# Performance work log

Measured on AMD Instinct MI355X. Metric: run time of the kernel, lower is better.

Reference implementation:

```python
import jax, jax.numpy as jnp
import numpy as np

VERY_NEG = -100000000000.0
EPS = 1e-10
PAGERANK_LAMBDA = 0.8
FACT_SCALE = 1.0
B, E, F, LQ = 64, 1000, 4000, 30
T = 100      # trans_units
EMB = 300    # embed_units
WV = 30000   # word vocab
EV = 50007   # entity vocab (+7 specials)
GNN_LAYERS = 2


def linear(x, W, b):
    return x @ W.T + b


def lstm(x, Wih, Whh, bih, bhh):
    # torch nn.LSTM, single layer, batch_first. gate order i,f,g,o
    Bb = x.shape[0]
    H = Whh.shape[1]
    def step(carry, xt):
        h, c = carry
        g = xt @ Wih.T + h @ Whh.T + bih + bhh
        i, f, gg, o = jnp.split(g, 4, axis=-1)
        c = jax.nn.sigmoid(f) * c + jax.nn.sigmoid(i) * jnp.tanh(gg)
        h = jax.nn.sigmoid(o) * jnp.tanh(c)
        return (h, c), h
    init = (jnp.zeros((Bb, H), x.dtype), jnp.zeros((Bb, H), x.dtype))
    (h, _), ys = jax.lax.scan(step, init, jnp.swapaxes(x, 0, 1))
    return jnp.swapaxes(ys, 0, 1), h


def gather_entity(x, head_idx):
    # sparse_bmm(entity2fact_mat, x): each fact row has one nonzero at its head entity
    # x [B,E,D], head_idx [B,F] -> [B,F,D]
    return jnp.take_along_axis(x, head_idx[:, :, None], axis=1)


def scatter_fact(y, tail_idx):
    # sparse_bmm(fact2entity_mat, y): scatter-add fact rows into their tail entity
    # y [B,F,D], tail_idx [B,F] -> [B,E,D]
    Bb, Ff, D = y.shape
    seg = (jnp.arange(Bb)[:, None] * E + tail_idx).reshape(-1)
    return jax.ops.segment_sum(y.reshape(Bb * Ff, D), seg, num_segments=Bb * E).reshape(Bb, E, D)


def forward(word_emb, entity_emb, ent_W, ent_b, lstm_Wih, lstm_Whh, lstm_bih, lstm_bhh,
            q2e_W, q2e_b, e2q_W, e2q_b, e2e_W, e2e_b,
            kbh_W, kbh_b, kbt_W, kbt_b, kbs_W, kbs_b,
            q2e_adj_mat, query_text, local_entity, kb_fact_rel, head_idx, tail_idx):
    div = jnp.sqrt(jnp.asarray(T, jnp.float32))
    query_mask = (query_text != 0).astype(jnp.float32)          # [B,LQ]

    # node encoder (LSTM) over query words
    qw = word_emb[query_text]                                   # [B,LQ,EMB]
    query_hidden_emb, qh = lstm(qw, lstm_Wih, lstm_Whh, lstm_bih, lstm_bhh)
    query_node_emb = qh[:, None, :]                             # [B,1,T]

    local_fact_emb = linear(entity_emb[kb_fact_rel], ent_W, ent_b)     # [B,F,T]
    local_entity_emb = linear(entity_emb[local_entity], ent_W, ent_b)  # [B,E,T]

    # fact <-> query attention (pre-GNN weighting)
    sim = jnp.einsum('blt,bft->blf', query_hidden_emb, local_fact_emb) / div
    sim = jax.nn.softmax(sim + (1.0 - query_mask[:, :, None]) * VERY_NEG, axis=1)
    fact2query_att = jnp.einsum('blf,blt->bft', sim, query_hidden_emb)  # [B,F,T]
    Wsc = jnp.sum(fact2query_att * local_fact_emb, axis=2) / div        # [B,F]
    W_tilde = jnp.exp(Wsc - jnp.max(Wsc, axis=1, keepdims=True))        # [B,F]

    # e2f_softmax = entity2fact^T @ W_tilde : per-entity sum of W_tilde over out-facts
    e2f_softmax = scatter_fact(W_tilde[:, :, None], head_idx)[:, :, 0]
    e2f_softmax = jnp.maximum(e2f_softmax, EPS)                         # [B,E]

    pagerank_f = q2e_adj_mat                                            # [B,E]
    for i in range(GNN_LAYERS):
        next_emb = local_entity_emb
        # question -> entity
        q2e = linear(jnp.broadcast_to(query_node_emb, (B, E, T)), q2e_W[i], q2e_b[i])
        next_emb = jnp.concatenate([next_emb, q2e], axis=2)
        # entity -> fact
        e2f_emb = jax.nn.relu(linear(local_fact_emb, kbs_W[i], kbs_b[i]) +
                              gather_entity(linear(local_entity_emb, kbh_W[i], kbh_b[i]), head_idx))
        e2f_norm = W_tilde[:, :, None] * gather_entity((pagerank_f / e2f_softmax)[:, :, None], head_idx)
        e2f_emb = e2f_emb * e2f_norm                                    # [B,F,T]
        # fact -> entity
        f2e_emb = jax.nn.relu(linear(local_entity_emb, kbs_W[i], kbs_b[i]) +
                              scatter_fact(linear(e2f_emb, kbt_W[i], kbt_b[i]), tail_idx))
        pagerank_f = (PAGERANK_LAMBDA * scatter_fact(e2f_norm, tail_idx)[:, :, 0] +
                      (1.0 - PAGERANK_LAMBDA) * pagerank_f)
        next_emb = jnp.concatenate([next_emb, FACT_SCALE * f2e_emb], axis=2)  # [B,E,3T]
        # entity -> query ; entity -> entity
        query_node_emb = jnp.einsum('be,bet->bt', pagerank_f,
                                    linear(next_emb, e2q_W[i], e2q_b[i]))[:, None, :]
        local_entity_emb = jax.nn.relu(linear(next_emb, e2e_W[i], e2e_b[i]))
    return local_entity_emb, query_node_emb, pagerank_f


def setup_inputs() -> dict:
    key = jax.random.key(0)
    ks = jax.random.split(key, 24)
    def n(k, shape, s=0.05):
        return (jax.random.normal(k, shape) * s).astype(jnp.float32)
    L, K3 = GNN_LAYERS, 3 * T
    inp = {}
    inp['word_emb'] = n(ks[0], (WV, EMB), 1.0)
    inp['entity_emb'] = n(ks[1], (EV, T), 1.0)
    inp['ent_W'] = n(ks[2], (T, T)); inp['ent_b'] = jnp.zeros((T,), jnp.float32)
    inp['lstm_Wih'] = n(ks[3], (4 * T, EMB)); inp['lstm_Whh'] = n(ks[4], (4 * T, T))
    inp['lstm_bih'] = jnp.zeros((4 * T,), jnp.float32)
    inp['lstm_bhh'] = jnp.zeros((4 * T,), jnp.float32)
    inp['q2e_W'] = n(ks[5], (L, T, T)); inp['q2e_b'] = jnp.zeros((L, T), jnp.float32)
    inp['e2q_W'] = n(ks[6], (L, T, K3)); inp['e2q_b'] = jnp.zeros((L, T), jnp.float32)
    inp['e2e_W'] = n(ks[7], (L, T, K3)); inp['e2e_b'] = jnp.zeros((L, T), jnp.float32)
    inp['kbh_W'] = n(ks[8], (L, T, T)); inp['kbh_b'] = jnp.zeros((L, T), jnp.float32)
    inp['kbt_W'] = n(ks[9], (L, T, T)); inp['kbt_b'] = jnp.zeros((L, T), jnp.float32)
    inp['kbs_W'] = n(ks[10], (L, T, T)); inp['kbs_b'] = jnp.zeros((L, T), jnp.float32)
    inp['q2e_adj_mat'] = (jax.random.uniform(ks[11], (B, E)) < 0.05).astype(jnp.float32)
    inp['query_text'] = jax.random.randint(ks[12], (B, LQ), 0, WV)
    inp['local_entity'] = jax.random.randint(ks[13], (B, E), 0, EV)
    inp['kb_fact_rel'] = jax.random.randint(ks[14], (B, F), 0, EV)
    inp['head_idx'] = jax.random.randint(ks[15], (B, F), 0, E)
    inp['tail_idx'] = jax.random.randint(ks[16], (B, F), 0, E)
    return inp


def reference(word_emb, entity_emb, ent_W, ent_b, lstm_Wih, lstm_Whh, lstm_bih, lstm_bhh,
              q2e_W, q2e_b, e2q_W, e2q_b, e2e_W, e2e_b,
              kbh_W, kbh_b, kbt_W, kbt_b, kbs_W, kbs_b,
              q2e_adj_mat, query_text, local_entity, kb_fact_rel, head_idx, tail_idx):
    return forward(word_emb, entity_emb, ent_W, ent_b, lstm_Wih, lstm_Whh, lstm_bih, lstm_bhh,
                   q2e_W, q2e_b, e2q_W, e2q_b, e2e_W, e2e_b,
                   kbh_W, kbh_b, kbt_W, kbt_b, kbs_W, kbs_b,
                   q2e_adj_mat, query_text, local_entity, kb_fact_rel, head_idx, tail_idx)
```

## Files before the change

kernel.cpp:

```cpp
#include <hip/hip_runtime.h>
#include <hip/hip_bf16.h>

#define BB 64
#define EE 1000
#define FF 4000
#define LQ_ 30
#define TT 100
#define EMB_ 300
#define G4 400
#define EV_ 50007
#define VERY_NEG_ (-100000000000.0f)
#define EPS_ 1e-10f

typedef __attribute__((ext_vector_type(8))) short bf16x8;
typedef __attribute__((ext_vector_type(4))) float f32x4;

__device__ __forceinline__ float sigm(float x) { return 1.0f / (1.0f + expf(-x)); }

__device__ __forceinline__ unsigned short f2bf(float v) {
    __hip_bfloat16 h = __float2bfloat16(v);
    return *reinterpret_cast<unsigned short*>(&h);
}
__device__ __forceinline__ float bf2f(unsigned short s) {
    return __uint_as_float((unsigned)s << 16);
}

__global__ void cvt_bf16_kernel(const float* __restrict__ in, unsigned short* __restrict__ out,
                                long n4) {
    long i = (long)blockIdx.x * 256 + threadIdx.x;
    if (i < n4) {
        float4 v = ((const float4*)in)[i];
        ushort4 o;
        o.x = f2bf(v.x); o.y = f2bf(v.y); o.z = f2bf(v.z); o.w = f2bf(v.w);
        ((ushort4*)out)[i] = o;
    }
}

__global__ void transpose_kernel(const float* __restrict__ in, float* __restrict__ out,
                                 int rows, int cols) {
    int i = blockIdx.x * 256 + threadIdx.x;
    if (i < rows * cols) {
        int r = i / cols, c = i % cols;
        out[c * rows + r] = in[i];
    }
}

__global__ __launch_bounds__(256)
void xw_kernel(const float* __restrict__ word_emb, const int* __restrict__ qtext,
               const float* __restrict__ WihT, const float* __restrict__ bih,
               const float* __restrict__ bhh, float* __restrict__ xw) {
    int bs0 = blockIdx.x * 4;
    __shared__ float x[4][EMB_];
    int tid = threadIdx.x;
    for (int i = tid; i < 4 * EMB_; i += 256) {
        int s = i / EMB_, k = i % EMB_;
        x[s][k] = word_emb[(long)qtext[bs0 + s] * EMB_ + k];
    }
    __syncthreads();
    for (int g = tid; g < G4; g += 256) {
        float b0 = bih[g] + bhh[g];
        float a0 = b0, a1 = b0, a2 = b0, a3 = b0;
        #pragma unroll 4
        for (int k = 0; k < EMB_; ++k) {
            float wv = WihT[k * G4 + g];
            a0 += x[0][k] * wv; a1 += x[1][k] * wv;
            a2 += x[2][k] * wv; a3 += x[3][k] * wv;
        }
        xw[(long)(bs0 + 0) * G4 + g] = a0;
        xw[(long)(bs0 + 1) * G4 + g] = a1;
        xw[(long)(bs0 + 2) * G4 + g] = a2;
        xw[(long)(bs0 + 3) * G4 + g] = a3;
    }
}

__global__ __launch_bounds__(512)
void lstm_kernel(const float* __restrict__ xw, const float* __restrict__ Whh,
                 float* __restrict__ qh_emb, float* __restrict__ qnode) {
    int b = blockIdx.x, tid = threadIdx.x;
    __shared__ __align__(16) float hs[TT];
    __shared__ float cs[TT];
    __shared__ float gs[G4];
    float4 w[25];
    if (tid < G4) {
        const float4* wr = (const float4*)(Whh + (long)tid * TT);
        #pragma unroll
        for (int j = 0; j < 25; ++j) w[j] = wr[j];
    }
    if (tid < TT) { hs[tid] = 0.f; cs[tid] = 0.f; }
    __syncthreads();
    for (int s = 0; s < LQ_; ++s) {
        if (tid < G4) {
            const float4* hv4 = (const float4*)hs;
            float a0 = 0.f, a1 = 0.f, a2 = 0.f, a3 = 0.f;
            #pragma unroll
            for (int j = 0; j < 25; ++j) {
                float4 hv = hv4[j];
                a0 += hv.x * w[j].x; a1 += hv.y * w[j].y;
                a2 += hv.z * w[j].z; a3 += hv.w * w[j].w;
            }
            gs[tid] = xw[((long)b * LQ_ + s) * G4 + tid] + (a0 + a1) + (a2 + a3);
        }
        __syncthreads();
        if (tid < TT) {
            float ci = sigm(gs[TT + tid]) * cs[tid] + sigm(gs[tid]) * tanhf(gs[2 * TT + tid]);
            float hi = sigm(gs[3 * TT + tid]) * tanhf(ci);
            cs[tid] = ci;
            hs[tid] = hi;
            qh_emb[((long)b * LQ_ + s) * TT + tid] = hi;
            if (s == LQ_ - 1) qnode[b * TT + tid] = hi;
        }
        __syncthreads();
    }
}

struct GOut {
    const float* W; int wstride;
    const float* bias;
    const float* bscale;
    const unsigned short* addb;
    const float* addf;
    const float* cvec;
    void* Y; int y_bf16; int relu;
};
struct GArgs {
    const void* X; int x_bf16;
    const int* gidx;
    long rows;
    int nw;
    GOut o[3];
};

__global__ __launch_bounds__(256)
void gemm_multi_kernel(GArgs a) {
    __shared__ __align__(16) short sX[64 * 136];
    __shared__ __align__(16) short sW[112 * 136];
    float* sOut = (float*)sW;
    int tid = threadIdx.x;
    long r0 = (long)blockIdx.x * 64;
    for (int i = tid; i < 64 * 25; i += 256) {
        int r = i / 25, c = i % 25;
        long rr = r0 + r;
        ushort4 v; v.x = 0; v.y = 0; v.z = 0; v.w = 0;
        if (rr < a.rows) {
            long xr = a.gidx ? (long)a.gidx[rr] : rr;
            if (a.x_bf16) {
                v = *(const ushort4*)((const unsigned short*)a.X + xr * TT + c * 4);
            } else {
                float4 f = *(const float4*)((const float*)a.X + xr * TT + c * 4);
                v.x = f2bf(f.x); v.y = f2bf(f.y); v.z = f2bf(f.z); v.w = f2bf(f.w);
            }
        }
        *(ushort4*)&sX[r * 136 + c * 4] = v;
    }
    for (int i = tid; i < 64 * 28; i += 256) {
        int r = i / 28, k = TT + i % 28;
        sX[r * 136 + k] = 0;
    }
    int lane = tid & 63, wv = tid >> 6;
    int arow = lane & 15, agrp = lane >> 4;
    int t_lo = lane & 15, r_hi = (lane >> 4) * 4;
    #pragma unroll
    for (int w = 0; w < 3; ++w) {
        if (w >= a.nw) break;
        for (int i = tid; i < 112 * 32; i += 256) {
            int t = i / 32, k = (i % 32) * 4;
            ushort4 v; v.x = 0; v.y = 0; v.z = 0; v.w = 0;
            if (t < TT && k < TT) {
                float4 f = *(const float4*)(a.o[w].W + (long)t * a.o[w].wstride + k);
                v.x = f2bf(f.x); v.y = f2bf(f.y); v.z = f2bf(f.z); v.w = f2bf(f.w);
            }
            *(ushort4*)&sW[t * 136 + k] = v;
        }
        __syncthreads();
        f32x4 acc[7];
        #pragma unroll
        for (int n = 0; n < 7; ++n) acc[n] = (f32x4){0.f, 0.f, 0.f, 0.f};
        #pragma unroll
        for (int kk = 0; kk < 4; ++kk) {
            bf16x8 av = *(const bf16x8*)&sX[(wv * 16 + arow) * 136 + kk * 32 + agrp * 8];
            #pragma unroll
            for (int n = 0; n < 7; ++n) {
                bf16x8 bv = *(const bf16x8*)&sW[(n * 16 + arow) * 136 + kk * 32 + agrp * 8];
                acc[n] = __builtin_amdgcn_mfma_f32_16x16x32_bf16(av, bv, acc[n], 0, 0, 0);
            }
        }
        __syncthreads();
        #pragma unroll
        for (int n = 0; n < 7; ++n) {
            int t = n * 16 + t_lo;
            if (t < TT) {
                #pragma unroll
                for (int j = 0; j < 4; ++j)
                    sOut[(wv * 16 + r_hi + j) * 104 + t] = acc[n][j];
            }
        }
        __syncthreads();
        for (int i = tid; i < 64 * 25; i += 256) {
            int r = i / 25, c = i % 25;
            long rr = r0 + r;
            if (rr < a.rows) {
                float4 v = *(float4*)&sOut[r * 104 + c * 4];
                if (a.o[w].bias) {
                    float bs = a.o[w].bscale ? a.o[w].bscale[rr] : 1.f;
                    float4 bv = *(const float4*)(a.o[w].bias + c * 4);
                    v.x += bv.x * bs; v.y += bv.y * bs; v.z += bv.z * bs; v.w += bv.w * bs;
                }
                if (a.o[w].addb) {
                    ushort4 ad = *(const ushort4*)(a.o[w].addb + rr * TT + c * 4);
                    v.x += bf2f(ad.x); v.y += bf2f(ad.y); v.z += bf2f(ad.z); v.w += bf2f(ad.w);
                }
                if (a.o[w].addf) {
                    float4 ad = *(const float4*)(a.o[w].addf + rr * TT + c * 4);
                    v.x += ad.x; v.y += ad.y; v.z += ad.z; v.w += ad.w;
                }
                if (a.o[w].cvec) {
                    float4 cv = *(const float4*)(a.o[w].cvec + (long)(rr / EE) * TT + c * 4);
                    v.x += cv.x; v.y += cv.y; v.z += cv.z; v.w += cv.w;
                }
                if (a.o[w].relu) {
                    v.x = fmaxf(v.x, 0.f); v.y = fmaxf(v.y, 0.f);
                    v.z = fmaxf(v.z, 0.f); v.w = fmaxf(v.w, 0.f);
                }
                if (a.o[w].y_bf16) {
                    ushort4 ov;
                    ov.x = f2bf(v.x); ov.y = f2bf(v.y); ov.z = f2bf(v.z); ov.w = f2bf(v.w);
                    *(ushort4*)((unsigned short*)a.o[w].Y + rr * TT + c * 4) = ov;
                } else {
                    *(float4*)((float*)a.o[w].Y + rr * TT + c * 4) = v;
                }
            }
        }
        __syncthreads();
    }
}

__global__ __launch_bounds__(128)
void compose_kernel(const float* __restrict__ A, const float* __restrict__ B,
                    const float* __restrict__ ab, const float* __restrict__ bb,
                    float* __restrict__ C, float* __restrict__ cb) {
    int i = blockIdx.x, j = threadIdx.x;
    __shared__ float arow[TT];
    if (j < TT) arow[j] = A[i * TT + j];
    __syncthreads();
    if (j < TT) {
        float acc = 0.f;
        for (int k = 0; k < TT; ++k) acc += arow[k] * B[k * TT + j];
        C[i * TT + j] = acc;
    }
    if (j == 0) {
        float acc = bb[i];
        for (int k = 0; k < TT; ++k) acc += arow[k] * ab[k];
        cb[i] = acc;
    }
}

__global__ __launch_bounds__(256)
void wsc_kernel(const float* __restrict__ qh_emb, const int* __restrict__ qtext,
                const unsigned short* __restrict__ ent_f, const int* __restrict__ rel,
                float* __restrict__ Wsc) {
    int b = blockIdx.x >> 4;
    int chunk = blockIdx.x & 15;
    __shared__ __align__(16) float qh[LQ_ * TT];
    __shared__ float msk[LQ_];
    for (int i = threadIdx.x; i < LQ_ * TT; i += 256) qh[i] = qh_emb[(long)b * LQ_ * TT + i];
    for (int i = threadIdx.x; i < LQ_; i += 256)
        msk[i] = (qtext[b * LQ_ + i] != 0) ? 0.f : VERY_NEG_;
    __syncthreads();
    int f = chunk * 256 + threadIdx.x;
    if (f >= FF) return;
    long bf = (long)b * FF + f;
    const unsigned short* fr = ent_f + (long)rel[bf] * TT;
    float sim[LQ_];
    #pragma unroll
    for (int l = 0; l < LQ_; ++l) sim[l] = 0.f;
    for (int kq = 0; kq < 25; ++kq) {
        ushort4 x4 = *(const ushort4*)(fr + kq * 4);
        float x0 = bf2f(x4.x), x1 = bf2f(x4.y), x2 = bf2f(x4.z), x3 = bf2f(x4.w);
        #pragma unroll
        for (int l = 0; l < LQ_; ++l) {
            float4 q = ((const float4*)(qh + l * TT))[kq];
            sim[l] += x0 * q.x + x1 * q.y + x2 * q.z + x3 * q.w;
        }
    }
    float mx = -INFINITY;
    #pragma unroll
    for (int l = 0; l < LQ_; ++l) {
        sim[l] *= 0.1f;
        mx = fmaxf(mx, sim[l] + msk[l]);
    }
    float ssum = 0.f, wsum = 0.f;
    #pragma unroll
    for (int l = 0; l < LQ_; ++l) {
        float p = expf(sim[l] + msk[l] - mx);
        ssum += p;
        wsum += p * sim[l];
    }
    Wsc[bf] = wsum / ssum;
}

__global__ __launch_bounds__(256)
void rowmax_kernel(const float* __restrict__ Wsc, float* __restrict__ bmax) {
    int b = blockIdx.x, tid = threadIdx.x;
    __shared__ float red[256];
    float m = -INFINITY;
    for (int f = tid; f < FF; f += 256) m = fmaxf(m, Wsc[(long)b * FF + f]);
    red[tid] = m;
    __syncthreads();
    for (int s = 128; s; s >>= 1) {
        if (tid < s) red[tid] = fmaxf(red[tid], red[tid + s]);
        __syncthreads();
    }
    if (tid == 0) bmax[b] = red[0];
}

__global__ __launch_bounds__(256)
void wtilde_kernel(const float* __restrict__ Wsc, const float* __restrict__ bmax,
                   const int* __restrict__ head, const int* __restrict__ tail,
                   float* __restrict__ W_tilde, float* __restrict__ e2f_sm,
                   float* __restrict__ cnt) {
    int idx = blockIdx.x * 256 + threadIdx.x;
    if (idx >= BB * FF) return;
    int b = idx / FF;
    float wt = expf(Wsc[idx] - bmax[b]);
    W_tilde[idx] = wt;
    atomicAdd(&e2f_sm[(long)b * EE + head[idx]], wt);
    atomicAdd(&cnt[(long)b * EE + tail[idx]], 1.f);
}

__global__ __launch_bounds__(128)
void qvec_kernel(const float* __restrict__ qnode,
                 const float* __restrict__ q2eW, const float* __restrict__ q2eb,
                 const float* __restrict__ e2eW, const float* __restrict__ e2eb,
                 const float* __restrict__ e2qW, const float* __restrict__ e2qb,
                 float* __restrict__ q2e_vec, float* __restrict__ cvec_e2e,
                 float* __restrict__ cvec_e2q) {
    int b = blockIdx.x, t = threadIdx.x;
    __shared__ float qn[TT], qv[TT];
    if (t < TT) qn[t] = qnode[b * TT + t];
    __syncthreads();
    if (t < TT) {
        float acc = q2eb[t];
        for (int k = 0; k < TT; ++k) acc += qn[k] * q2eW[t * TT + k];
        qv[t] = acc;
        q2e_vec[b * TT + t] = acc;
    }
    __syncthreads();
    if (t < TT) {
        float a1 = e2eb[t], a2 = e2qb[t];
        for (int k = 0; k < TT; ++k) {
            a1 += qv[k] * e2eW[(long)t * 300 + TT + k];
            a2 += qv[k] * e2qW[(long)t * 300 + TT + k];
        }
        cvec_e2e[b * TT + t] = a1;
        cvec_e2q[b * TT + t] = a2;
    }
}

__global__ __launch_bounds__(256)
void norm_kernel(const float* __restrict__ W_tilde, const float* __restrict__ pr,
                 const float* __restrict__ e2f_sm, const int* __restrict__ head,
                 const int* __restrict__ tail, float* __restrict__ norm,
                 float* __restrict__ pr_acc) {
    int idx = blockIdx.x * 256 + threadIdx.x;
    if (idx >= BB * FF) return;
    int b = idx / FF;
    int h = head[idx];
    float n = W_tilde[idx] * pr[(long)b * EE + h] / fmaxf(e2f_sm[(long)b * EE + h], EPS_);
    norm[idx] = n;
    if (n != 0.f) atomicAdd(&pr_acc[(long)b * EE + tail[idx]], n);
}

__global__ __launch_bounds__(256)
void e2f_elem_kernel(const unsigned short* __restrict__ ent_kbs,
                     const unsigned short* __restrict__ kbh,
                     const float* __restrict__ norm, const int* __restrict__ rel,
                     const int* __restrict__ head, const int* __restrict__ tail,
                     float* __restrict__ eacc) {
    long idx = (long)blockIdx.x * 256 + threadIdx.x;
    if (idx >= (long)BB * FF * 25) return;
    int q = (int)(idx % 25);
    long bf = idx / 25;
    int b = (int)(bf / FF);
    float n = norm[bf];
    if (n == 0.f) return;
    ushort4 s4 = *(const ushort4*)(ent_kbs + (long)rel[bf] * TT + q * 4);
    ushort4 k4 = *(const ushort4*)(kbh + ((long)b * EE + head[bf]) * TT + q * 4);
    float* dst = eacc + ((long)b * EE + tail[bf]) * TT + q * 4;
    atomicAdd(dst + 0, fmaxf(bf2f(s4.x) + bf2f(k4.x), 0.f) * n);
    atomicAdd(dst + 1, fmaxf(bf2f(s4.y) + bf2f(k4.y), 0.f) * n);
    atomicAdd(dst + 2, fmaxf(bf2f(s4.z) + bf2f(k4.z), 0.f) * n);
    atomicAdd(dst + 3, fmaxf(bf2f(s4.w) + bf2f(k4.w), 0.f) * n);
}

__global__ void pr_update_kernel(const float* __restrict__ pr_acc, float* __restrict__ pr,
                                 float* __restrict__ out2) {
    int i = blockIdx.x * 256 + threadIdx.x;
    if (i < BB * EE) {
        float v = 0.8f * pr_acc[i] + 0.2f * pr[i];
        pr[i] = v;
        if (out2) out2[i] = v;
    }
}

#define RCH 50
__global__ __launch_bounds__(128)
void reduce_kernel(const float* __restrict__ pr, const unsigned short* __restrict__ ent,
                   const int* __restrict__ gidx, const unsigned short* __restrict__ f2e,
                   float* __restrict__ s1, float* __restrict__ s3, float* __restrict__ prsum) {
    int b = blockIdx.x / (EE / RCH), ch = blockIdx.x % (EE / RCH);
    int e0 = ch * RCH, tid = threadIdx.x;
    __shared__ float prl[RCH];
    __shared__ long erow[RCH];
    if (tid < RCH) {
        long idx = (long)b * EE + e0 + tid;
        prl[tid] = pr[idx];
        erow[tid] = gidx ? (long)gidx[idx] : idx;
    }
    __syncthreads();
    if (tid == 0) {
        float s = 0.f;
        for (int e = 0; e < RCH; ++e) s += prl[e];
        if (s != 0.f) atomicAdd(&prsum[b], s);
    }
    if (tid < TT) {
        float a1 = 0.f, a3 = 0.f;
        for (int e = 0; e < RCH; ++e) {
            float p = prl[e];
            if (p != 0.f) {
                a1 += p * bf2f(ent[erow[e] * TT + tid]);
                a3 += p * bf2f(f2e[((long)b * EE + e0 + e) * TT + tid]);
            }
        }
        atomicAdd(&s1[b * TT + tid], a1);
        atomicAdd(&s3[b * TT + tid], a3);
    }
}

__global__ __launch_bounds__(128)
void qnode_kernel(const float* __restrict__ s1, const float* __restrict__ s3,
                  const float* __restrict__ prsum, const float* __restrict__ cvec_e2q,
                  const float* __restrict__ e2qW, float* __restrict__ qnode,
                  float* __restrict__ out2) {
    int b = blockIdx.x, t = threadIdx.x;
    __shared__ float s1l[TT], s3l[TT];
    if (t < TT) { s1l[t] = s1[b * TT + t]; s3l[t] = s3[b * TT + t]; }
    __syncthreads();
    if (t < TT) {
        float acc = prsum[b] * cvec_e2q[b * TT + t];
        const float* wr = e2qW + (long)t * 300;
        for (int k = 0; k < TT; ++k) acc += s1l[k] * wr[k] + s3l[k] * wr[200 + k];
        qnode[b * TT + t] = acc;
        if (out2) out2[b * TT + t] = acc;
    }
}

extern "C" void kernel_launch(void* const* d_in, const int* in_sizes, int n_in,
                              void* d_out, int out_size, void* d_ws, size_t ws_size,
                              hipStream_t stream) {
    const float* word_emb   = (const float*)d_in[0];
    const float* entity_emb = (const float*)d_in[1];
    const float* ent_W      = (const float*)d_in[2];
    const float* ent_b      = (const float*)d_in[3];
    const float* lstm_Wih   = (const float*)d_in[4];
    const float* lstm_Whh   = (const float*)d_in[5];
    const float* lstm_bih   = (const float*)d_in[6];
    const float* lstm_bhh   = (const float*)d_in[7];
    const float* q2e_W      = (const float*)d_in[8];
    const float* q2e_b      = (const float*)d_in[9];
    const float* e2q_W      = (const float*)d_in[10];
    const float* e2q_b      = (const float*)d_in[11];
    const float* e2e_W      = (const float*)d_in[12];
    const float* e2e_b      = (const float*)d_in[13];
    const float* kbh_W      = (const float*)d_in[14];
    const float* kbh_b      = (const float*)d_in[15];
    const float* kbt_W      = (const float*)d_in[16];
    const float* kbt_b      = (const float*)d_in[17];
    const float* kbs_W      = (const float*)d_in[18];
    const float* kbs_b      = (const float*)d_in[19];
    const float* q2e_adj    = (const float*)d_in[20];
    const int* query_text   = (const int*)d_in[21];
    const int* local_entity = (const int*)d_in[22];
    const int* kb_fact_rel  = (const int*)d_in[23];
    const int* head_idx     = (const int*)d_in[24];
    const int* tail_idx     = (const int*)d_in[25];
    float* out = (float*)d_out;

    char* base = (char*)d_ws;
    size_t off = 0;
    auto alloc = [&](size_t bytes) {
        void* p = base + off;
        off = (off + bytes + 255) & ~(size_t)255;
        return p;
    };
    const size_t NE = (size_t)BB * EE;
    unsigned short* emb_bf  = (unsigned short*)alloc((size_t)EV_ * TT * 2);
    unsigned short* ent_f   = (unsigned short*)alloc((size_t)EV_ * TT * 2);
    unsigned short* kbs0    = (unsigned short*)alloc((size_t)EV_ * TT * 2);
    unsigned short* kbs1    = (unsigned short*)alloc((size_t)EV_ * TT * 2);
    unsigned short* entB    = (unsigned short*)alloc(NE * TT * 2);
    unsigned short* kbh_bf  = (unsigned short*)alloc(NE * TT * 2);
    unsigned short* kbs_e   = (unsigned short*)alloc(NE * TT * 2);
    float* tmp              = (float*)alloc(NE * TT * 4);
    float* eacc             = (float*)alloc(NE * TT * 4);
    float* pr_acc           = (float*)alloc(NE * 4);
    float* xw               = (float*)alloc((size_t)BB * LQ_ * G4 * 4);
    float* qh_emb           = (float*)alloc((size_t)BB * LQ_ * TT * 4);
    float* WihT             = (float*)alloc((size_t)G4 * EMB_ * 4);
    float* Wsc              = (float*)alloc((size_t)BB * FF * 4);
    float* W_tilde          = (float*)alloc((size_t)BB * FF * 4);
    float* normf            = (float*)alloc((size_t)BB * FF * 4);
    float* bmaxb            = (float*)alloc(BB * 4);
    float* e2f_sm           = (float*)alloc(NE * 4);
    float* cnt              = (float*)alloc(NE * 4);
    float* pr               = (float*)alloc(NE * 4);
    float* qnode            = (float*)alloc((size_t)BB * TT * 4);
    float* q2e_vec          = (float*)alloc((size_t)BB * TT * 4);
    float* cvec_e2e         = (float*)alloc((size_t)BB * TT * 4);
    float* cvec_e2q         = (float*)alloc((size_t)BB * TT * 4);
    float* s1               = (float*)alloc((size_t)BB * TT * 4);
    float* s3               = (float*)alloc((size_t)BB * TT * 4);
    float* prsum            = (float*)alloc(BB * 4);
    float* Ckbs0            = (float*)alloc((size_t)TT * TT * 4);
    float* Ckbs1            = (float*)alloc((size_t)TT * TT * 4);
    float* cb0              = (float*)alloc(TT * 4);
    float* cb1              = (float*)alloc(TT * 4);
    unsigned short* f2e = kbh_bf;

    transpose_kernel<<<(G4 * EMB_ + 255) / 256, 256, 0, stream>>>(lstm_Wih, WihT, G4, EMB_);
    xw_kernel<<<BB * LQ_ / 4, 256, 0, stream>>>(word_emb, query_text, WihT, lstm_bih, lstm_bhh, xw);
    lstm_kernel<<<BB, 512, 0, stream>>>(xw, lstm_Whh, qh_emb, qnode);

    cvt_bf16_kernel<<<(EV_ * TT / 4 + 255) / 256, 256, 0, stream>>>(entity_emb, emb_bf,
                                                                    (long)EV_ * TT / 4);
    compose_kernel<<<TT, 128, 0, stream>>>(kbs_W, ent_W, ent_b, kbs_b, Ckbs0, cb0);
    compose_kernel<<<TT, 128, 0, stream>>>(kbs_W + TT * TT, ent_W, ent_b, kbs_b + TT,
                                           Ckbs1, cb1);
    {
        GArgs g{};
        g.X = emb_bf; g.x_bf16 = 1; g.gidx = nullptr; g.rows = EV_; g.nw = 3;
        g.o[0].W = ent_W; g.o[0].wstride = TT; g.o[0].bias = ent_b;
        g.o[0].Y = ent_f; g.o[0].y_bf16 = 1;
        g.o[1].W = Ckbs0; g.o[1].wstride = TT; g.o[1].bias = cb0;
        g.o[1].Y = kbs0; g.o[1].y_bf16 = 1;
        g.o[2].W = Ckbs1; g.o[2].wstride = TT; g.o[2].bias = cb1;
        g.o[2].Y = kbs1; g.o[2].y_bf16 = 1;
        gemm_multi_kernel<<<(EV_ + 63) / 64, 256, 0, stream>>>(g);
    }

    wsc_kernel<<<BB * 16, 256, 0, stream>>>(qh_emb, query_text, ent_f, kb_fact_rel, Wsc);
    rowmax_kernel<<<BB, 256, 0, stream>>>(Wsc, bmaxb);
    hipMemsetAsync(e2f_sm, 0, 2 * NE * 4, stream);
    wtilde_kernel<<<(BB * FF + 255) / 256, 256, 0, stream>>>(Wsc, bmaxb, head_idx, tail_idx,
                                                             W_tilde, e2f_sm, cnt);
    hipMemcpyAsync(pr, q2e_adj, NE * 4, hipMemcpyDeviceToDevice, stream);

    for (int i = 0; i < 2; ++i) {
        const unsigned short* kbs_tab = i ? kbs1 : kbs0;
        qvec_kernel<<<BB, 128, 0, stream>>>(qnode, q2e_W + i * TT * TT, q2e_b + i * TT,
                                            e2e_W + i * TT * 300, e2e_b + i * TT,
                                            e2q_W + i * TT * 300, e2q_b + i * TT,
                                            q2e_vec, cvec_e2e, cvec_e2q);
        {
            GArgs g{};
            g.X = i ? (const void*)entB : (const void*)ent_f;
            g.x_bf16 = 1;
            g.gidx = i ? nullptr : local_entity;
            g.rows = (long)NE; g.nw = 3;
            g.o[0].W = kbh_W + i * TT * TT; g.o[0].wstride = TT; g.o[0].bias = kbh_b + i * TT;
            g.o[0].Y = kbh_bf; g.o[0].y_bf16 = 1;
            g.o[1].W = kbs_W + i * TT * TT; g.o[1].wstride = TT; g.o[1].bias = kbs_b + i * TT;
            g.o[1].Y = kbs_e; g.o[1].y_bf16 = 1;
            g.o[2].W = e2e_W + i * TT * 300; g.o[2].wstride = 300;
            g.o[2].Y = tmp; g.o[2].y_bf16 = 0;
            gemm_multi_kernel<<<(int)(NE / 64), 256, 0, stream>>>(g);
        }
        hipMemsetAsync(eacc, 0, NE * TT * 4 + NE * 4, stream);
        norm_kernel<<<(BB * FF + 255) / 256, 256, 0, stream>>>(W_tilde, pr, e2f_sm, head_idx,
                                                               tail_idx, normf, pr_acc);
        e2f_elem_kernel<<<(int)(((long)BB * FF * 25 + 255) / 256), 256, 0, stream>>>(
            kbs_tab, kbh_bf, normf, kb_fact_rel, head_idx, tail_idx, eacc);
        {
            GArgs g{};
            g.X = eacc; g.x_bf16 = 0; g.gidx = nullptr; g.rows = (long)NE; g.nw = 1;
            g.o[0].W = kbt_W + i * TT * TT; g.o[0].wstride = TT;
            g.o[0].bias = kbt_b + i * TT; g.o[0].bscale = cnt;
            g.o[0].addb = kbs_e;
            g.o[0].Y = (void*)f2e; g.o[0].y_bf16 = 1; g.o[0].relu = 1;
            gemm_multi_kernel<<<(int)(NE / 64), 256, 0, stream>>>(g);
        }
        pr_update_kernel<<<(int)((NE + 255) / 256), 256, 0, stream>>>(
            pr_acc, pr, (i == 1) ? out + 6406400 : nullptr);
        hipMemsetAsync(s1, 0, (size_t)(2 * BB * TT + BB) * 4, stream);
        reduce_kernel<<<BB * (EE / RCH), 128, 0, stream>>>(
            pr, i ? entB : ent_f, i ? nullptr : local_entity, f2e, s1, s3, prsum);
        qnode_kernel<<<BB, 128, 0, stream>>>(s1, s3, prsum, cvec_e2q, e2q_W + i * TT * 300,
                                             qnode, (i == 1) ? out + 6400000 : nullptr);
        {
            GArgs g{};
            g.X = f2e; g.x_bf16 = 1; g.gidx = nullptr; g.rows = (long)NE; g.nw = 1;
            g.o[0].W = e2e_W + i * TT * 300 + 200; g.o[0].wstride = 300;
            g.o[0].addf = tmp; g.o[0].cvec = cvec_e2e; g.o[0].relu = 1;
            g.o[0].Y = i ? (void*)out : (void*)entB; g.o[0].y_bf16 = i ? 0 : 1;
            gemm_multi_kernel<<<(int)(NE / 64), 256, 0, stream>>>(g);
        }
    }
}
```

Measured before the change: 831.1 us.

## Replace atomic fact scatter with tail-sorted CSR gather and bf16 intermediates

Builds a per-batch CSR of facts grouped by tail entity once (prefix scan plus counting-sort permutation). The two message-passing layers then use a gather kernel where each entity accumulates its incoming facts in registers and writes the result once. This removes the large float atomicAdd scatter, the eacc memset and the separate norm kernel. The e2e partial and the accumulated messages are also stored as bf16 instead of fp32, which halves that traffic but loses some precision. Within-bin fact order is nondeterministic, and work is uneven across bins.

```diff
diff --git a/kernel.cpp b/kernel.cpp
--- a/kernel.cpp
+++ b/kernel.cpp
@@ -327,69 +327,73 @@
     atomicAdd(&cnt[(long)b * EE + tail[idx]], 1.f);
 }
 
-__global__ __launch_bounds__(128)
-void qvec_kernel(const float* __restrict__ qnode,
-                 const float* __restrict__ q2eW, const float* __restrict__ q2eb,
-                 const float* __restrict__ e2eW, const float* __restrict__ e2eb,
-                 const float* __restrict__ e2qW, const float* __restrict__ e2qb,
-                 float* __restrict__ q2e_vec, float* __restrict__ cvec_e2e,
-                 float* __restrict__ cvec_e2q) {
-    int b = blockIdx.x, t = threadIdx.x;
-    __shared__ float qn[TT], qv[TT];
-    if (t < TT) qn[t] = qnode[b * TT + t];
-    __syncthreads();
-    if (t < TT) {
-        float acc = q2eb[t];
-        for (int k = 0; k < TT; ++k) acc += qn[k] * q2eW[t * TT + k];
-        qv[t] = acc;
-        q2e_vec[b * TT + t] = acc;
-    }
-    __syncthreads();
-    if (t < TT) {
-        float a1 = e2eb[t], a2 = e2qb[t];
-        for (int k = 0; k < TT; ++k) {
-            a1 += qv[k] * e2eW[(long)t * 300 + TT + k];
-            a2 += qv[k] * e2qW[(long)t * 300 + TT + k];
-        }
-        cvec_e2e[b * TT + t] = a1;
-        cvec_e2q[b * TT + t] = a2;
-    }
-}
-
-__global__ __launch_bounds__(256)
-void norm_kernel(const float* __restrict__ W_tilde, const float* __restrict__ pr,
-                 const float* __restrict__ e2f_sm, const int* __restrict__ head,
-                 const int* __restrict__ tail, float* __restrict__ norm,
-                 float* __restrict__ pr_acc) {
+__global__ __launch_bounds__(256)
+void scan_kernel(const float* __restrict__ cnt, int* __restrict__ offs) {
+    int b = blockIdx.x, tid = threadIdx.x;
+    __shared__ int ls[256];
+    int c0 = 0, c1 = 0, c2 = 0, c3 = 0;
+    int start = tid * 4;
+    if (start + 0 < EE) c0 = (int)cnt[(long)b * EE + start + 0];
+    if (start + 1 < EE) c1 = (int)cnt[(long)b * EE + start + 1];
+    if (start + 2 < EE) c2 = (int)cnt[(long)b * EE + start + 2];
+    if (start + 3 < EE) c3 = (int)cnt[(long)b * EE + start + 3];
+    int s = c0 + c1 + c2 + c3;
+    ls[tid] = s;
+    __syncthreads();
+    for (int d = 1; d < 256; d <<= 1) {
+        int v = (tid >= d) ? ls[tid - d] : 0;
+        __syncthreads();
+        ls[tid] += v;
+        __syncthreads();
+    }
+    int excl = ls[tid] - s + b * FF;
+    if (start + 0 < EE) { offs[(long)b * EE + start + 0] = excl; excl += c0; }
+    if (start + 1 < EE) { offs[(long)b * EE + start + 1] = excl; excl += c1; }
+    if (start + 2 < EE) { offs[(long)b * EE + start + 2] = excl; excl += c2; }
+    if (start + 3 < EE) { offs[(long)b * EE + start + 3] = excl; excl += c3; }
+    if (b == BB - 1 && tid == 255) offs[BB * EE] = BB * FF;
+}
+
+__global__ __launch_bounds__(256)
+void sortfacts_kernel(const int* __restrict__ tail, const int* __restrict__ offs,
+                      int* __restrict__ fillc, int* __restrict__ perm) {
     int idx = blockIdx.x * 256 + threadIdx.x;
     if (idx >= BB * FF) return;
     int b = idx / FF;
-    int h = head[idx];
-    float n = W_tilde[idx] * pr[(long)b * EE + h] / fmaxf(e2f_sm[(long)b * EE + h], EPS_);
-    norm[idx] = n;
-    if (n != 0.f) atomicAdd(&pr_acc[(long)b * EE + tail[idx]], n);
-}
-
-__global__ __launch_bounds__(256)
-void e2f_elem_kernel(const unsigned short* __restrict__ ent_kbs,
-                     const unsigned short* __restrict__ kbh,
-                     const float* __restrict__ norm, const int* __restrict__ rel,
-                     const int* __restrict__ head, const int* __restrict__ tail,
-                     float* __restrict__ eacc) {
-    long idx = (long)blockIdx.x * 256 + threadIdx.x;
-    if (idx >= (long)BB * FF * 25) return;
-    int q = (int)(idx % 25);
-    long bf = idx / 25;
-    int b = (int)(bf / FF);
-    float n = norm[bf];
-    if (n == 0.f) return;
-    ushort4 s4 = *(const ushort4*)(ent_kbs + (long)rel[bf] * TT + q * 4);
-    ushort4 k4 = *(const ushort4*)(kbh + ((long)b * EE + head[bf]) * TT + q * 4);
-    float* dst = eacc + ((long)b * EE + tail[bf]) * TT + q * 4;
-    atomicAdd(dst + 0, fmaxf(bf2f(s4.x) + bf2f(k4.x), 0.f) * n);
-    atomicAdd(dst + 1, fmaxf(bf2f(s4.y) + bf2f(k4.y), 0.f) * n);
-    atomicAdd(dst + 2, fmaxf(bf2f(s4.z) + bf2f(k4.z), 0.f) * n);
-    atomicAdd(dst + 3, fmaxf(bf2f(s4.w) + bf2f(k4.w), 0.f) * n);
+    int bin = b * EE + tail[idx];
+    int pos = offs[bin] + atomicAdd(&fillc[bin], 1);
+    perm[pos] = idx;
+}
+
+__global__ __launch_bounds__(256)
+void e2f_sorted_kernel(const unsigned short* __restrict__ kbs_tab,
+                       const unsigned short* __restrict__ kbh,
+                       const float* __restrict__ W_tilde, const float* __restrict__ pr,
+                       const float* __restrict__ e2f_sm,
+                       const int* __restrict__ rel, const int* __restrict__ head,
+                       const int* __restrict__ offs, const int* __restrict__ perm,
+                       unsigned short* __restrict__ eaccb, float* __restrict__ pr_acc) {
+    int grp = threadIdx.x >> 7;
+    int t = threadIdx.x & 127;
+    int bin = blockIdx.x * 2 + grp;
+    if (bin >= BB * EE) return;
+    int b = bin / EE;
+    int j0 = offs[bin], j1 = offs[bin + 1];
+    float acc = 0.f, nsum = 0.f;
+    for (int j = j0; j < j1; ++j) {
+        int f = perm[j];
+        long bh = (long)b * EE + head[f];
+        float n = W_tilde[f] * pr[bh] / fmaxf(e2f_sm[bh], EPS_);
+        if (n != 0.f) {
+            nsum += n;
+            if (t < TT) {
+                float v = bf2f(kbs_tab[(long)rel[f] * TT + t]) + bf2f(kbh[bh * TT + t]);
+                acc += fmaxf(v, 0.f) * n;
+            }
+        }
+    }
+    if (t < TT) eaccb[(long)bin * TT + t] = f2bf(acc);
+    if (t == TT) pr_acc[bin] = nsum;
 }
 
 __global__ void pr_update_kernel(const float* __restrict__ pr_acc, float* __restrict__ pr,
@@ -433,6 +437,35 @@
         }
         atomicAdd(&s1[b * TT + tid], a1);
         atomicAdd(&s3[b * TT + tid], a3);
+    }
+}
+
+__global__ __launch_bounds__(128)
+void qvec_kernel(const float* __restrict__ qnode,
+                 const float* __restrict__ q2eW, const float* __restrict__ q2eb,
+                 const float* __restrict__ e2eW, const float* __restrict__ e2eb,
+                 const float* __restrict__ e2qW, const float* __restrict__ e2qb,
+                 float* __restrict__ q2e_vec, float* __restrict__ cvec_e2e,
+                 float* __restrict__ cvec_e2q) {
+    int b = blockIdx.x, t = threadIdx.x;
+    __shared__ float qn[TT], qv[TT];
+    if (t < TT) qn[t] = qnode[b * TT + t];
+    __syncthreads();
+    if (t < TT) {
+        float acc = q2eb[t];
+        for (int k = 0; k < TT; ++k) acc += qn[k] * q2eW[t * TT + k];
+        qv[t] = acc;
+        q2e_vec[b * TT + t] = acc;
+    }
+    __syncthreads();
+    if (t < TT) {
+        float a1 = e2eb[t], a2 = e2qb[t];
+        for (int k = 0; k < TT; ++k) {
+            a1 += qv[k] * e2eW[(long)t * 300 + TT + k];
+            a2 += qv[k] * e2qW[(long)t * 300 + TT + k];
+        }
+        cvec_e2e[b * TT + t] = a1;
+        cvec_e2q[b * TT + t] = a2;
     }
 }
 
@@ -500,15 +533,14 @@
     unsigned short* entB    = (unsigned short*)alloc(NE * TT * 2);
     unsigned short* kbh_bf  = (unsigned short*)alloc(NE * TT * 2);
     unsigned short* kbs_e   = (unsigned short*)alloc(NE * TT * 2);
-    float* tmp              = (float*)alloc(NE * TT * 4);
-    float* eacc             = (float*)alloc(NE * TT * 4);
+    unsigned short* tmp     = (unsigned short*)alloc(NE * TT * 2);
+    unsigned short* eaccb   = (unsigned short*)alloc(NE * TT * 2);
     float* pr_acc           = (float*)alloc(NE * 4);
     float* xw               = (float*)alloc((size_t)BB * LQ_ * G4 * 4);
     float* qh_emb           = (float*)alloc((size_t)BB * LQ_ * TT * 4);
     float* WihT             = (float*)alloc((size_t)G4 * EMB_ * 4);
     float* Wsc              = (float*)alloc((size_t)BB * FF * 4);
     float* W_tilde          = (float*)alloc((size_t)BB * FF * 4);
-    float* normf            = (float*)alloc((size_t)BB * FF * 4);
     float* bmaxb            = (float*)alloc(BB * 4);
     float* e2f_sm           = (float*)alloc(NE * 4);
     float* cnt              = (float*)alloc(NE * 4);
@@ -524,6 +556,9 @@
     float* Ckbs1            = (float*)alloc((size_t)TT * TT * 4);
     float* cb0              = (float*)alloc(TT * 4);
     float* cb1              = (float*)alloc(TT * 4);
+    int* offs               = (int*)alloc((NE + 1) * 4);
+    int* fillc              = (int*)alloc(NE * 4);
+    int* perm               = (int*)alloc((size_t)BB * FF * 4);
     unsigned short* f2e = kbh_bf;
 
     transpose_kernel<<<(G4 * EMB_ + 255) / 256, 256, 0, stream>>>(lstm_Wih, WihT, G4, EMB_);
@@ -553,6 +588,10 @@
     wtilde_kernel<<<(BB * FF + 255) / 256, 256, 0, stream>>>(Wsc, bmaxb, head_idx, tail_idx,
                                                              W_tilde, e2f_sm, cnt);
     hipMemcpyAsync(pr, q2e_adj, NE * 4, hipMemcpyDeviceToDevice, stream);
+
+    scan_kernel<<<BB, 256, 0, stream>>>(cnt, offs);
+    hipMemsetAsync(fillc, 0, NE * 4, stream);
+    sortfacts_kernel<<<(BB * FF + 255) / 256, 256, 0, stream>>>(tail_idx, offs, fillc, perm);
 
     for (int i = 0; i < 2; ++i) {
         const unsigned short* kbs_tab = i ? kbs1 : kbs0;
@@ -571,17 +610,15 @@
             g.o[1].W = kbs_W + i * TT * TT; g.o[1].wstride = TT; g.o[1].bias = kbs_b + i * TT;
             g.o[1].Y = kbs_e; g.o[1].y_bf16 = 1;
             g.o[2].W = e2e_W + i * TT * 300; g.o[2].wstride = 300;
-            g.o[2].Y = tmp; g.o[2].y_bf16 = 0;
+            g.o[2].Y = tmp; g.o[2].y_bf16 = 1;
             gemm_multi_kernel<<<(int)(NE / 64), 256, 0, stream>>>(g);
         }
-        hipMemsetAsync(eacc, 0, NE * TT * 4 + NE * 4, stream);
-        norm_kernel<<<(BB * FF + 255) / 256, 256, 0, stream>>>(W_tilde, pr, e2f_sm, head_idx,
-                                                               tail_idx, normf, pr_acc);
-        e2f_elem_kernel<<<(int)(((long)BB * FF * 25 + 255) / 256), 256, 0, stream>>>(
-            kbs_tab, kbh_bf, normf, kb_fact_rel, head_idx, tail_idx, eacc);
+        e2f_sorted_kernel<<<(int)(NE / 2), 256, 0, stream>>>(
+            kbs_tab, kbh_bf, W_tilde, pr, e2f_sm, kb_fact_rel, head_idx, offs, perm,
+            eaccb, pr_acc);
         {
             GArgs g{};
-            g.X = eacc; g.x_bf16 = 0; g.gidx = nullptr; g.rows = (long)NE; g.nw = 1;
+            g.X = eaccb; g.x_bf16 = 1; g.gidx = nullptr; g.rows = (long)NE; g.nw = 1;
             g.o[0].W = kbt_W + i * TT * TT; g.o[0].wstride = TT;
             g.o[0].bias = kbt_b + i * TT; g.o[0].bscale = cnt;
             g.o[0].addb = kbs_e;
@@ -599,7 +636,7 @@
             GArgs g{};
             g.X = f2e; g.x_bf16 = 1; g.gidx = nullptr; g.rows = (long)NE; g.nw = 1;
             g.o[0].W = e2e_W + i * TT * 300 + 200; g.o[0].wstride = 300;
-            g.o[0].addf = tmp; g.o[0].cvec = cvec_e2e; g.o[0].relu = 1;
+            g.o[0].addb = tmp; g.o[0].cvec = cvec_e2e; g.o[0].relu = 1;
             g.o[0].Y = i ? (void*)out : (void*)entB; g.o[0].y_bf16 = i ? 0 : 1;
             gemm_multi_kernel<<<(int)(NE / 64), 256, 0, stream>>>(g);
         }
```

Result: no change. 844.4 us (+1.6%).
